# Optimization experiments

Hardware: AMD Instinct MI355X
Metric: run time of the kernel (lower is better)

## Reference

```python
import jax, jax.numpy as jnp
import numpy as np

E = 16          # num_experts
H = 2048        # hidden_size
I = 768         # moe_intermediate_size
T = 2048        # tokens (batch*seq)
K = 2           # top_k


def setup_inputs() -> dict:
    key = jax.random.key(0)
    k1, k2, k3, k4, k5 = jax.random.split(key, 5)
    hidden_states = jax.random.normal(k1, (T, H), dtype=jnp.float32)
    top_k_index = jax.random.randint(k2, (T, K), 0, E, dtype=jnp.int32)
    w = jax.random.uniform(k3, (T, K), dtype=jnp.float32)
    top_k_weights = w / jnp.sum(w, axis=-1, keepdims=True)  # softmax-like router weights
    init_std = 0.02
    gate_up_proj = jax.random.normal(k4, (E, 2 * I, H), dtype=jnp.float32) * init_std
    down_proj = jax.random.normal(k5, (E, H, I), dtype=jnp.float32) * init_std
    return {
        "hidden_states": hidden_states,
        "top_k_index": top_k_index,
        "top_k_weights": top_k_weights,
        "gate_up_proj": gate_up_proj,
        "down_proj": down_proj,
    }


def reference(hidden_states, top_k_index, top_k_weights, gate_up_proj, down_proj):
    # Combine matrix C[t, e] = sum_k top_k_weights[t, k] * 1[top_k_index[t,k] == e]
    # Tokens not routed to expert e get weight 0, so the dense-masked compute
    # below is mathematically identical to the per-expert gather/scatter loop.
    t_idx = jnp.arange(T)[:, None]
    C = jnp.zeros((T, E), dtype=hidden_states.dtype).at[t_idx, top_k_index].add(top_k_weights)

    # gate/up projection for every (token, expert): [T, E, 2I]
    gu = jnp.einsum('th,egh->teg', hidden_states, gate_up_proj)
    gate, up = jnp.split(gu, 2, axis=-1)                  # [T, E, I] each
    mid = jax.nn.silu(gate) * up                          # SwiGLU, [T, E, I]
    # down projection fused with routed combine weights -> [T, H]
    out = jnp.einsum('tei,ehi,te->th', mid, down_proj, C)
    return out
```

## Files before the change

### kernel.cpp

```cpp
#include <hip/hip_runtime.h>

#define TTOK  2048
#define HID   2048
#define IMID  768
#define NEXP  16
#define NPAIR 4096
#define NSLOT 4224
#define BM    128
#define BK    64
#define MAXT  48
#define ABUF  (128 * 64)

#define HS_U   524288u
#define GUP_U  6291456u
#define DN_U   3145728u
#define NU_TOT (HS_U + GUP_U + DN_U)

typedef __attribute__((ext_vector_type(8))) short  short8;
typedef __attribute__((ext_vector_type(4))) float  floatx4;

__device__ __forceinline__ unsigned pk2(float a, float b) {
    union { float f; unsigned u; } x{a}, y{b};
    unsigned ra = (x.u + 0x7FFFu + ((x.u >> 16) & 1u)) >> 16;
    unsigned rb = (y.u + 0x7FFFu + ((y.u >> 16) & 1u)) & 0xFFFF0000u;
    return ra | rb;
}

__device__ __forceinline__ short f2bf(float f) {
    union { float f; unsigned u; } v; v.f = f;
    return (short)((v.u + 0x7FFFu + ((v.u >> 16) & 1u)) >> 16);
}

__device__ __forceinline__ short8 cvt8(float4 a, float4 b) {
    union { unsigned u[4]; short8 s; } r;
    r.u[0] = pk2(a.x, a.y); r.u[1] = pk2(a.z, a.w);
    r.u[2] = pk2(b.x, b.y); r.u[3] = pk2(b.z, b.w);
    return r.s;
}

__device__ __forceinline__ void async_cp16(const void* g, void* l) {
    __builtin_amdgcn_global_load_lds(
        (const __attribute__((address_space(1))) void*)g,
        (__attribute__((address_space(3))) void*)l, 16, 0, 0);
}

__global__ __launch_bounds__(256) void k_pre(
    const float* __restrict__ hs, const int* __restrict__ idx,
    const float* __restrict__ tkw, const float* __restrict__ gup,
    const float* __restrict__ down, int* __restrict__ ntiles,
    int4* __restrict__ tiles, int* __restrict__ tok,
    float* __restrict__ wgt, short* __restrict__ X,
    short* __restrict__ gupb, short* __restrict__ downb)
{
    const int tid = threadIdx.x;
    if (blockIdx.x == 0) {
        __shared__ int cnt[NEXP], cur[NEXP];
        if (tid < NEXP) cnt[tid] = 0;
        __syncthreads();
        for (int i = tid; i < NPAIR; i += 256) atomicAdd(&cnt[idx[i]], 1);
        __syncthreads();
        if (tid == 0) {
            int s = 0, nt = 0;
            for (int e = 0; e < NEXP; e++) {
                cur[e] = s;
                int n = cnt[e];
                for (int tt = 0; tt * BM < n; tt++) {
                    tiles[nt] = make_int4(e, s + tt * BM, min(BM, n - tt * BM), 0);
                    nt++;
                }
                s += n;
            }
            *ntiles = nt;
        }
        __syncthreads();
        for (int i = tid; i < NPAIR; i += 256) {
            int e = idx[i];
            int p = atomicAdd(&cur[e], 1);
            tok[p] = i >> 1;
            wgt[p] = tkw[i];
        }
        for (int i = NPAIR + tid; i < NSLOT; i += 256) { tok[i] = 0; wgt[i] = 0.0f; }
        return;
    }
    const unsigned nthr = (gridDim.x - 1) * 256u;
    unsigned u = (blockIdx.x - 1) * 256u + tid;
    for (; u < NU_TOT; u += nthr) {
        const float* src; short* dst; unsigned off;
        if (u < HS_U)              { src = hs;   dst = X;     off = u; }
        else if (u < HS_U + GUP_U) { src = gup;  dst = gupb;  off = u - HS_U; }
        else                       { src = down; dst = downb; off = u - HS_U - GUP_U; }
        float4 a = *((const float4*)src + (size_t)2 * off);
        float4 b = *((const float4*)src + (size_t)2 * off + 1);
        *((short8*)dst + off) = cvt8(a, b);
    }
}

__global__ __launch_bounds__(256, 2) void k_gemm1(
    const short* __restrict__ gupb, const short* __restrict__ X,
    const int* __restrict__ ntiles, const int4* __restrict__ tiles,
    const int* __restrict__ tok, const float* __restrict__ wgt,
    short* __restrict__ mid)
{
    if ((int)blockIdx.y >= *ntiles) return;
    const int4 td = tiles[blockIdx.y];
    const int e = td.x, rowstart = td.y, nvalid = td.z;
    const int ct = blockIdx.x;

    __shared__ short sA[2 * ABUF];
    __shared__ short sB[2 * ABUF];
    __shared__ int   s_tok[BM];
    __shared__ float s_w[BM];

    const int tid = threadIdx.x;
    if (tid < BM) { s_tok[tid] = tok[rowstart + tid]; s_w[tid] = wgt[rowstart + tid]; }
    __syncthreads();

    const int wave = tid >> 6, lane = tid & 63;
    const int m16 = lane & 15, quad = lane >> 4;

    const int lrow = tid >> 3;
    const int gsw  = (tid & 7) ^ (lrow & 7);
    const short* aga[4];
    const short* bga[4];
#pragma unroll
    for (int j = 0; j < 4; j++)
        aga[j] = X + (size_t)s_tok[lrow + j * 32] * HID + gsw * 8;
    const short* gb = gupb + (size_t)e * (2 * IMID) * HID + gsw * 8;
#pragma unroll
    for (int j = 0; j < 2; j++) {
        bga[j]     = gb + (size_t)(ct * 64 + lrow + j * 32) * HID;
        bga[j + 2] = gb + (size_t)(IMID + ct * 64 + lrow + j * 32) * HID;
    }

    auto stage = [&](int k0, short* dA, short* dB) {
#pragma unroll
        for (int j = 0; j < 4; j++)
            async_cp16(aga[j] + k0, dA + j * 2048 + wave * 512);
#pragma unroll
        for (int j = 0; j < 4; j++)
            async_cp16(bga[j] + k0, dB + j * 2048 + wave * 512);
    };

    const int Wm = (wave >> 1) << 6;
    const int Wi = (wave & 1) << 5;
    floatx4 ag[4][2], au[4][2];
#pragma unroll
    for (int a = 0; a < 4; a++)
#pragma unroll
        for (int b = 0; b < 2; b++) { ag[a][b] = (floatx4)0.0f; au[a][b] = (floatx4)0.0f; }

    stage(0, sA, sB);

    const int nsteps = HID / BK;
    for (int ks = 0; ks < nsteps; ks++) {
        const short* Acur = sA + (ks & 1) * ABUF;
        const short* Bcur = sB + (ks & 1) * ABUF;
        if (ks + 1 < nsteps) {
            stage((ks + 1) * BK, sA + ((ks + 1) & 1) * ABUF, sB + ((ks + 1) & 1) * ABUF);
            asm volatile("s_waitcnt vmcnt(8)" ::: "memory");
        } else {
            asm volatile("s_waitcnt vmcnt(0)" ::: "memory");
        }
        __builtin_amdgcn_s_barrier();
        __builtin_amdgcn_sched_barrier(0);

#pragma unroll
        for (int h = 0; h < 2; h++) {
            short8 af[4];
#pragma unroll
            for (int mf = 0; mf < 4; mf++) {
                int row = Wm + mf * 16 + m16;
                int gc = (h * 4 + quad) ^ (row & 7);
                af[mf] = *(const short8*)&Acur[row * 64 + gc * 8];
            }
#pragma unroll
            for (int nf = 0; nf < 2; nf++) {
                int brow = Wi + nf * 16 + m16;
                int gcb = (h * 4 + quad) ^ (brow & 7);
                const short8 bg = *(const short8*)&Bcur[brow * 64 + gcb * 8];
                const short8 bu = *(const short8*)&Bcur[(64 + brow) * 64 + gcb * 8];
#pragma unroll
                for (int mf = 0; mf < 4; mf++) {
                    ag[mf][nf] = __builtin_amdgcn_mfma_f32_16x16x32_bf16(af[mf], bg, ag[mf][nf], 0, 0, 0);
                    au[mf][nf] = __builtin_amdgcn_mfma_f32_16x16x32_bf16(af[mf], bu, au[mf][nf], 0, 0, 0);
                }
            }
        }
        __builtin_amdgcn_sched_barrier(0);
        __builtin_amdgcn_s_barrier();
    }

#pragma unroll
    for (int mf = 0; mf < 4; mf++) {
#pragma unroll
        for (int r = 0; r < 4; r++) {
            int m = Wm + mf * 16 + quad * 4 + r;
            if (m < nvalid) {
                float w = s_w[m];
                size_t rowp = (size_t)(rowstart + m) * IMID + ct * 64;
#pragma unroll
                for (int nf = 0; nf < 2; nf++) {
                    float g = ag[mf][nf][r], u = au[mf][nf][r];
                    float val = g / (1.0f + __expf(-g)) * u * w;
                    mid[rowp + Wi + nf * 16 + m16] = f2bf(val);
                }
            }
        }
    }
}

__global__ __launch_bounds__(256, 2) void k_gemm2(
    const short* __restrict__ downb, const short* __restrict__ mid,
    const int* __restrict__ ntiles, const int4* __restrict__ tiles,
    const int* __restrict__ tok, float* __restrict__ out)
{
    if ((int)blockIdx.y >= *ntiles) return;
    const int4 td = tiles[blockIdx.y];
    const int e = td.x, rowstart = td.y, nvalid = td.z;
    const int ct = blockIdx.x;

    __shared__ short sA[2 * ABUF];
    __shared__ short sB[2 * ABUF];
    __shared__ int   s_tok[BM];

    const int tid = threadIdx.x;
    if (tid < BM) s_tok[tid] = tok[rowstart + tid];
    __syncthreads();

    const int wave = tid >> 6, lane = tid & 63;
    const int m16 = lane & 15, quad = lane >> 4;

    const int lrow = tid >> 3;
    const int gsw  = (tid & 7) ^ (lrow & 7);
    const short* aga[4];
    const short* bga[4];
#pragma unroll
    for (int j = 0; j < 4; j++)
        aga[j] = mid + (size_t)(rowstart + lrow + j * 32) * IMID + gsw * 8;
    const short* db = downb + ((size_t)e * HID + ct * 128) * IMID + gsw * 8;
#pragma unroll
    for (int j = 0; j < 4; j++)
        bga[j] = db + (size_t)(lrow + j * 32) * IMID;

    auto stage = [&](int k0, short* dA, short* dB) {
#pragma unroll
        for (int j = 0; j < 4; j++)
            async_cp16(aga[j] + k0, dA + j * 2048 + wave * 512);
#pragma unroll
        for (int j = 0; j < 4; j++)
            async_cp16(bga[j] + k0, dB + j * 2048 + wave * 512);
    };

    const int Wm = (wave >> 1) << 6;
    const int Wn = (wave & 1) << 6;
    floatx4 acc[4][4];
#pragma unroll
    for (int a = 0; a < 4; a++)
#pragma unroll
        for (int b = 0; b < 4; b++) acc[a][b] = (floatx4)0.0f;

    stage(0, sA, sB);

    const int nsteps = IMID / BK;
    for (int ks = 0; ks < nsteps; ks++) {
        const short* Acur = sA + (ks & 1) * ABUF;
        const short* Bcur = sB + (ks & 1) * ABUF;
        if (ks + 1 < nsteps) {
            stage((ks + 1) * BK, sA + ((ks + 1) & 1) * ABUF, sB + ((ks + 1) & 1) * ABUF);
            asm volatile("s_waitcnt vmcnt(8)" ::: "memory");
        } else {
            asm volatile("s_waitcnt vmcnt(0)" ::: "memory");
        }
        __builtin_amdgcn_s_barrier();
        __builtin_amdgcn_sched_barrier(0);

#pragma unroll
        for (int h = 0; h < 2; h++) {
            short8 af[4];
#pragma unroll
            for (int mf = 0; mf < 4; mf++) {
                int row = Wm + mf * 16 + m16;
                int gc = (h * 4 + quad) ^ (row & 7);
                af[mf] = *(const short8*)&Acur[row * 64 + gc * 8];
            }
#pragma unroll
            for (int nf = 0; nf < 4; nf++) {
                int brow = Wn + nf * 16 + m16;
                int gcb = (h * 4 + quad) ^ (brow & 7);
                const short8 bf_ = *(const short8*)&Bcur[brow * 64 + gcb * 8];
#pragma unroll
                for (int mf = 0; mf < 4; mf++)
                    acc[mf][nf] = __builtin_amdgcn_mfma_f32_16x16x32_bf16(af[mf], bf_, acc[mf][nf], 0, 0, 0);
            }
        }
        __builtin_amdgcn_sched_barrier(0);
        __builtin_amdgcn_s_barrier();
    }

#pragma unroll
    for (int mf = 0; mf < 4; mf++) {
#pragma unroll
        for (int r = 0; r < 4; r++) {
            int m = Wm + mf * 16 + quad * 4 + r;
            if (m < nvalid) {
                int t = s_tok[m];
                float* op = out + (size_t)t * HID + ct * 128;
#pragma unroll
                for (int nf = 0; nf < 4; nf++)
                    atomicAdd(op + Wn + nf * 16 + m16, acc[mf][nf][r]);
            }
        }
    }
}

extern "C" void kernel_launch(void* const* d_in, const int* in_sizes, int n_in,
                              void* d_out, int out_size, void* d_ws, size_t ws_size,
                              hipStream_t stream) {
    const float* hs   = (const float*)d_in[0];
    const int*   idx  = (const int*)d_in[1];
    const float* tkw  = (const float*)d_in[2];
    const float* gup  = (const float*)d_in[3];
    const float* down = (const float*)d_in[4];
    float* out = (float*)d_out;

    char* ws = (char*)d_ws;
    int*   ntiles = (int*)ws;
    int4*  tiles  = (int4*)(ws + 16);
    int*   tok    = (int*)(ws + 1024);
    float* wgt    = (float*)(ws + 1024 + NSLOT * 4);
    short* mid    = (short*)(ws + 36864);
    short* X      = (short*)(ws + 36864 + (size_t)NSLOT * IMID * 2);
    short* gupb   = (short*)(ws + (16u << 20));
    short* downb  = (short*)(ws + (16u << 20) + (size_t)NEXP * 2 * IMID * HID * 2);

    hipMemsetAsync(d_out, 0, (size_t)TTOK * HID * sizeof(float), stream);
    k_pre  <<<2049, 256, 0, stream>>>(
        hs, idx, tkw, gup, down, ntiles, tiles, tok, wgt, X, gupb, downb);
    k_gemm1<<<dim3(IMID / 64, MAXT), 256, 0, stream>>>(gupb, X, ntiles, tiles, tok, wgt, mid);
    k_gemm2<<<dim3(HID / 128, MAXT), 256, 0, stream>>>(downb, mid, ntiles, tiles, tok, out);
}
```

Baseline: 476.5 us.

## Use 4-stage BK=32 async LDS pipeline with single barrier per step

Both expert GEMMs switch from a double-buffered BK=64 loop to a four-slot ring of BK=32 stages. Three stages stay in flight and only one barrier is issued per step. The XOR swizzle on the LDS layout is dropped for a plain 32-wide row layout. The fp32-to-bf16 prepass now converts one float4 per thread iteration instead of two. The deeper prefetch is meant to hide global-load latency better, at the cost of more barriers per K and possible LDS bank conflicts without the swizzle.

```diff
diff --git a/kernel.cpp b/kernel.cpp
--- a/kernel.cpp
+++ b/kernel.cpp
@@ -7,35 +7,21 @@
 #define NPAIR 4096
 #define NSLOT 4224
 #define BM    128
-#define BK    64
 #define MAXT  48
-#define ABUF  (128 * 64)
-
-#define HS_U   524288u
-#define GUP_U  6291456u
-#define DN_U   3145728u
-#define NU_TOT (HS_U + GUP_U + DN_U)
+#define HBUF  4096
+
+#define HS4   1048576u
+#define GUP4  12582912u
+#define DN4   6291456u
+#define N4TOT (HS4 + GUP4 + DN4)
 
 typedef __attribute__((ext_vector_type(8))) short  short8;
+typedef __attribute__((ext_vector_type(4))) short  bfx4;
 typedef __attribute__((ext_vector_type(4))) float  floatx4;
-
-__device__ __forceinline__ unsigned pk2(float a, float b) {
-    union { float f; unsigned u; } x{a}, y{b};
-    unsigned ra = (x.u + 0x7FFFu + ((x.u >> 16) & 1u)) >> 16;
-    unsigned rb = (y.u + 0x7FFFu + ((y.u >> 16) & 1u)) & 0xFFFF0000u;
-    return ra | rb;
-}
 
 __device__ __forceinline__ short f2bf(float f) {
     union { float f; unsigned u; } v; v.f = f;
     return (short)((v.u + 0x7FFFu + ((v.u >> 16) & 1u)) >> 16);
-}
-
-__device__ __forceinline__ short8 cvt8(float4 a, float4 b) {
-    union { unsigned u[4]; short8 s; } r;
-    r.u[0] = pk2(a.x, a.y); r.u[1] = pk2(a.z, a.w);
-    r.u[2] = pk2(b.x, b.y); r.u[3] = pk2(b.z, b.w);
-    return r.s;
 }
 
 __device__ __forceinline__ void async_cp16(const void* g, void* l) {
@@ -83,15 +69,15 @@
         return;
     }
     const unsigned nthr = (gridDim.x - 1) * 256u;
-    unsigned u = (blockIdx.x - 1) * 256u + tid;
-    for (; u < NU_TOT; u += nthr) {
-        const float* src; short* dst; unsigned off;
-        if (u < HS_U)              { src = hs;   dst = X;     off = u; }
-        else if (u < HS_U + GUP_U) { src = gup;  dst = gupb;  off = u - HS_U; }
-        else                       { src = down; dst = downb; off = u - HS_U - GUP_U; }
-        float4 a = *((const float4*)src + (size_t)2 * off);
-        float4 b = *((const float4*)src + (size_t)2 * off + 1);
-        *((short8*)dst + off) = cvt8(a, b);
+    for (unsigned u = (blockIdx.x - 1) * 256u + tid; u < N4TOT; u += nthr) {
+        const float4* s; bfx4* d; unsigned off;
+        if (u < HS4)              { s = (const float4*)hs;   d = (bfx4*)X;     off = u; }
+        else if (u < HS4 + GUP4)  { s = (const float4*)gup;  d = (bfx4*)gupb;  off = u - HS4; }
+        else                      { s = (const float4*)down; d = (bfx4*)downb; off = u - HS4 - GUP4; }
+        float4 v = s[off];
+        bfx4 o;
+        o.x = f2bf(v.x); o.y = f2bf(v.y); o.z = f2bf(v.z); o.w = f2bf(v.w);
+        d[off] = o;
     }
 }
 
@@ -106,8 +92,8 @@
     const int e = td.x, rowstart = td.y, nvalid = td.z;
     const int ct = blockIdx.x;
 
-    __shared__ short sA[2 * ABUF];
-    __shared__ short sB[2 * ABUF];
+    __shared__ short sA[4 * HBUF];
+    __shared__ short sB[4 * HBUF];
     __shared__ int   s_tok[BM];
     __shared__ float s_w[BM];
 
@@ -118,27 +104,21 @@
     const int wave = tid >> 6, lane = tid & 63;
     const int m16 = lane & 15, quad = lane >> 4;
 
-    const int lrow = tid >> 3;
-    const int gsw  = (tid & 7) ^ (lrow & 7);
-    const short* aga[4];
-    const short* bga[4];
-#pragma unroll
-    for (int j = 0; j < 4; j++)
-        aga[j] = X + (size_t)s_tok[lrow + j * 32] * HID + gsw * 8;
-    const short* gb = gupb + (size_t)e * (2 * IMID) * HID + gsw * 8;
-#pragma unroll
-    for (int j = 0; j < 2; j++) {
-        bga[j]     = gb + (size_t)(ct * 64 + lrow + j * 32) * HID;
-        bga[j + 2] = gb + (size_t)(IMID + ct * 64 + lrow + j * 32) * HID;
-    }
-
-    auto stage = [&](int k0, short* dA, short* dB) {
-#pragma unroll
-        for (int j = 0; j < 4; j++)
-            async_cp16(aga[j] + k0, dA + j * 2048 + wave * 512);
-#pragma unroll
-        for (int j = 0; j < 4; j++)
-            async_cp16(bga[j] + k0, dB + j * 2048 + wave * 512);
+    const int srow = wave * 16 + (lane >> 2);
+    const int kch  = (lane & 3) * 8;
+    const short* aga0 = X + (size_t)s_tok[srow]      * HID + kch;
+    const short* aga1 = X + (size_t)s_tok[srow + 64] * HID + kch;
+    const short* bga0 = gupb + ((size_t)e * (2 * IMID) + ct * 64 + srow) * HID + kch;
+    const short* bga1 = gupb + ((size_t)e * (2 * IMID) + IMID + ct * 64 + srow) * HID + kch;
+
+    auto stage = [&](int h) {
+        short* dA = sA + (h & 3) * HBUF;
+        short* dB = sB + (h & 3) * HBUF;
+        const int k0 = h * 32;
+        async_cp16(aga0 + k0, dA + wave * 512);
+        async_cp16(aga1 + k0, dA + 2048 + wave * 512);
+        async_cp16(bga0 + k0, dB + wave * 512);
+        async_cp16(bga1 + k0, dB + 2048 + wave * 512);
     };
 
     const int Wm = (wave >> 1) << 6;
@@ -149,46 +129,46 @@
 #pragma unroll
         for (int b = 0; b < 2; b++) { ag[a][b] = (floatx4)0.0f; au[a][b] = (floatx4)0.0f; }
 
-    stage(0, sA, sB);
-
-    const int nsteps = HID / BK;
-    for (int ks = 0; ks < nsteps; ks++) {
-        const short* Acur = sA + (ks & 1) * ABUF;
-        const short* Bcur = sB + (ks & 1) * ABUF;
-        if (ks + 1 < nsteps) {
-            stage((ks + 1) * BK, sA + ((ks + 1) & 1) * ABUF, sB + ((ks + 1) & 1) * ABUF);
-            asm volatile("s_waitcnt vmcnt(8)" ::: "memory");
-        } else {
-            asm volatile("s_waitcnt vmcnt(0)" ::: "memory");
-        }
+    auto mfma_phase = [&](int c) {
+        const short* A = sA + c * HBUF;
+        const short* B = sB + c * HBUF;
+        short8 af[4];
+#pragma unroll
+        for (int mf = 0; mf < 4; mf++)
+            af[mf] = *(const short8*)&A[(Wm + mf * 16 + m16) * 32 + quad * 8];
+#pragma unroll
+        for (int nf = 0; nf < 2; nf++) {
+            const short8 bg = *(const short8*)&B[(Wi + nf * 16 + m16) * 32 + quad * 8];
+            const short8 bu = *(const short8*)&B[(64 + Wi + nf * 16 + m16) * 32 + quad * 8];
+#pragma unroll
+            for (int mf = 0; mf < 4; mf++) {
+                ag[mf][nf] = __builtin_amdgcn_mfma_f32_16x16x32_bf16(af[mf], bg, ag[mf][nf], 0, 0, 0);
+                au[mf][nf] = __builtin_amdgcn_mfma_f32_16x16x32_bf16(af[mf], bu, au[mf][nf], 0, 0, 0);
+            }
+        }
+    };
+
+    const int nh = HID / 32;
+    stage(0); stage(1); stage(2);
+    for (int h = 0; h < nh - 3; ++h) {
+        asm volatile("s_waitcnt vmcnt(8)" ::: "memory");
         __builtin_amdgcn_s_barrier();
         __builtin_amdgcn_sched_barrier(0);
-
-#pragma unroll
-        for (int h = 0; h < 2; h++) {
-            short8 af[4];
-#pragma unroll
-            for (int mf = 0; mf < 4; mf++) {
-                int row = Wm + mf * 16 + m16;
-                int gc = (h * 4 + quad) ^ (row & 7);
-                af[mf] = *(const short8*)&Acur[row * 64 + gc * 8];
-            }
-#pragma unroll
-            for (int nf = 0; nf < 2; nf++) {
-                int brow = Wi + nf * 16 + m16;
-                int gcb = (h * 4 + quad) ^ (brow & 7);
-                const short8 bg = *(const short8*)&Bcur[brow * 64 + gcb * 8];
-                const short8 bu = *(const short8*)&Bcur[(64 + brow) * 64 + gcb * 8];
-#pragma unroll
-                for (int mf = 0; mf < 4; mf++) {
-                    ag[mf][nf] = __builtin_amdgcn_mfma_f32_16x16x32_bf16(af[mf], bg, ag[mf][nf], 0, 0, 0);
-                    au[mf][nf] = __builtin_amdgcn_mfma_f32_16x16x32_bf16(af[mf], bu, au[mf][nf], 0, 0, 0);
-                }
-            }
-        }
-        __builtin_amdgcn_sched_barrier(0);
-        __builtin_amdgcn_s_barrier();
-    }
+        stage(h + 3);
+        mfma_phase(h & 3);
+    }
+    asm volatile("s_waitcnt vmcnt(8)" ::: "memory");
+    __builtin_amdgcn_s_barrier();
+    __builtin_amdgcn_sched_barrier(0);
+    mfma_phase((nh - 3) & 3);
+    asm volatile("s_waitcnt vmcnt(4)" ::: "memory");
+    __builtin_amdgcn_s_barrier();
+    __builtin_amdgcn_sched_barrier(0);
+    mfma_phase((nh - 2) & 3);
+    asm volatile("s_waitcnt vmcnt(0)" ::: "memory");
+    __builtin_amdgcn_s_barrier();
+    __builtin_amdgcn_sched_barrier(0);
+    mfma_phase((nh - 1) & 3);
 
 #pragma unroll
     for (int mf = 0; mf < 4; mf++) {
@@ -219,8 +199,8 @@
     const int e = td.x, rowstart = td.y, nvalid = td.z;
     const int ct = blockIdx.x;
 
-    __shared__ short sA[2 * ABUF];
-    __shared__ short sB[2 * ABUF];
+    __shared__ short sA[4 * HBUF];
+    __shared__ short sB[4 * HBUF];
     __shared__ int   s_tok[BM];
 
     const int tid = threadIdx.x;
@@ -230,25 +210,21 @@
     const int wave = tid >> 6, lane = tid & 63;
     const int m16 = lane & 15, quad = lane >> 4;
 
-    const int lrow = tid >> 3;
-    const int gsw  = (tid & 7) ^ (lrow & 7);
-    const short* aga[4];
-    const short* bga[4];
-#pragma unroll
-    for (int j = 0; j < 4; j++)
-        aga[j] = mid + (size_t)(rowstart + lrow + j * 32) * IMID + gsw * 8;
-    const short* db = downb + ((size_t)e * HID + ct * 128) * IMID + gsw * 8;
-#pragma unroll
-    for (int j = 0; j < 4; j++)
-        bga[j] = db + (size_t)(lrow + j * 32) * IMID;
-
-    auto stage = [&](int k0, short* dA, short* dB) {
-#pragma unroll
-        for (int j = 0; j < 4; j++)
-            async_cp16(aga[j] + k0, dA + j * 2048 + wave * 512);
-#pragma unroll
-        for (int j = 0; j < 4; j++)
-            async_cp16(bga[j] + k0, dB + j * 2048 + wave * 512);
+    const int srow = wave * 16 + (lane >> 2);
+    const int kch  = (lane & 3) * 8;
+    const short* aga0 = mid + (size_t)(rowstart + srow)      * IMID + kch;
+    const short* aga1 = mid + (size_t)(rowstart + srow + 64) * IMID + kch;
+    const short* bga0 = downb + ((size_t)e * HID + ct * 128 + srow) * IMID + kch;
+    const short* bga1 = downb + ((size_t)e * HID + ct * 128 + 64 + srow) * IMID + kch;
+
+    auto stage = [&](int h) {
+        short* dA = sA + (h & 3) * HBUF;
+        short* dB = sB + (h & 3) * HBUF;
+        const int k0 = h * 32;
+        async_cp16(aga0 + k0, dA + wave * 512);
+        async_cp16(aga1 + k0, dA + 2048 + wave * 512);
+        async_cp16(bga0 + k0, dB + wave * 512);
+        async_cp16(bga1 + k0, dB + 2048 + wave * 512);
     };
 
     const int Wm = (wave >> 1) << 6;
@@ -259,43 +235,43 @@
 #pragma unroll
         for (int b = 0; b < 4; b++) acc[a][b] = (floatx4)0.0f;
 
-    stage(0, sA, sB);
-
-    const int nsteps = IMID / BK;
-    for (int ks = 0; ks < nsteps; ks++) {
-        const short* Acur = sA + (ks & 1) * ABUF;
-        const short* Bcur = sB + (ks & 1) * ABUF;
-        if (ks + 1 < nsteps) {
-            stage((ks + 1) * BK, sA + ((ks + 1) & 1) * ABUF, sB + ((ks + 1) & 1) * ABUF);
-            asm volatile("s_waitcnt vmcnt(8)" ::: "memory");
-        } else {
-            asm volatile("s_waitcnt vmcnt(0)" ::: "memory");
-        }
+    auto mfma_phase = [&](int c) {
+        const short* A = sA + c * HBUF;
+        const short* B = sB + c * HBUF;
+        short8 af[4];
+#pragma unroll
+        for (int mf = 0; mf < 4; mf++)
+            af[mf] = *(const short8*)&A[(Wm + mf * 16 + m16) * 32 + quad * 8];
+#pragma unroll
+        for (int nf = 0; nf < 4; nf++) {
+            const short8 bf_ = *(const short8*)&B[(Wn + nf * 16 + m16) * 32 + quad * 8];
+#pragma unroll
+            for (int mf = 0; mf < 4; mf++)
+                acc[mf][nf] = __builtin_amdgcn_mfma_f32_16x16x32_bf16(af[mf], bf_, acc[mf][nf], 0, 0, 0);
+        }
+    };
+
+    const int nh = IMID / 32;
+    stage(0); stage(1); stage(2);
+    for (int h = 0; h < nh - 3; ++h) {
+        asm volatile("s_waitcnt vmcnt(8)" ::: "memory");
         __builtin_amdgcn_s_barrier();
         __builtin_amdgcn_sched_barrier(0);
-
-#pragma unroll
-        for (int h = 0; h < 2; h++) {
-            short8 af[4];
-#pragma unroll
-            for (int mf = 0; mf < 4; mf++) {
-                int row = Wm + mf * 16 + m16;
-                int gc = (h * 4 + quad) ^ (row & 7);
-                af[mf] = *(const short8*)&Acur[row * 64 + gc * 8];
-            }
-#pragma unroll
-            for (int nf = 0; nf < 4; nf++) {
-                int brow = Wn + nf * 16 + m16;
-                int gcb = (h * 4 + quad) ^ (brow & 7);
-                const short8 bf_ = *(const short8*)&Bcur[brow * 64 + gcb * 8];
-#pragma unroll
-                for (int mf = 0; mf < 4; mf++)
-                    acc[mf][nf] = __builtin_amdgcn_mfma_f32_16x16x32_bf16(af[mf], bf_, acc[mf][nf], 0, 0, 0);
-            }
-        }
-        __builtin_amdgcn_sched_barrier(0);
-        __builtin_amdgcn_s_barrier();
-    }
+        stage(h + 3);
+        mfma_phase(h & 3);
+    }
+    asm volatile("s_waitcnt vmcnt(8)" ::: "memory");
+    __builtin_amdgcn_s_barrier();
+    __builtin_amdgcn_sched_barrier(0);
+    mfma_phase((nh - 3) & 3);
+    asm volatile("s_waitcnt vmcnt(4)" ::: "memory");
+    __builtin_amdgcn_s_barrier();
+    __builtin_amdgcn_sched_barrier(0);
+    mfma_phase((nh - 2) & 3);
+    asm volatile("s_waitcnt vmcnt(0)" ::: "memory");
+    __builtin_amdgcn_s_barrier();
+    __builtin_amdgcn_sched_barrier(0);
+    mfma_phase((nh - 1) & 3);
 
 #pragma unroll
     for (int mf = 0; mf < 4; mf++) {
```

After: 492.2 us. 3.3% more time.
